# Performance work log

Hardware: AMD Instinct MI355X
Metric: run time of the kernel (lower is better)

The kernel has to match this reference:

```python
import jax, jax.numpy as jnp
import numpy as np

_CODESZ = 8   # E8 codeword dimension
_OFFSET = 0.25  # half-integer shift applied to D8 points


def _build_grid():
    # Faithful replication of get_grid(): cartesian product of arange(-4,4)
    # over 8 dims (torch.cartesian_prod order == 'ij' meshgrid, last dim fastest),
    # keep points with even coordinate sum and squared norm <= 10 (D8 subset),
    # then concat [d8 - 1/4, d8 + 1/4]. Yields 55650 codewords of dim 8.
    rng = np.arange(-4, 4, dtype=np.int8)
    pts = np.stack(np.meshgrid(*([rng] * _CODESZ), indexing='ij'), axis=-1).reshape(-1, _CODESZ)
    s = pts.sum(axis=-1, dtype=np.int16)
    n2 = (pts.astype(np.int16) * pts).sum(axis=-1)  # max 8*16 fits int16
    d8 = pts[(s % 2 == 0) & (n2 <= 10)].astype(np.float32)  # [27825, 8]
    grid = np.concatenate([d8 - _OFFSET, d8 + _OFFSET], axis=0)  # [55650, 8]
    grid_norm = (grid * grid).sum(axis=-1)  # diag(grid @ grid.T), [55650]
    return jnp.asarray(grid), jnp.asarray(grid_norm)


def setup_inputs() -> dict:
    key = jax.random.key(0)
    X = jax.random.normal(key, (8192, _CODESZ), dtype=jnp.float32)
    grid, grid_norm = _build_grid()
    return {"X": X, "grid": grid, "grid_norm": grid_norm}


def reference(X, grid, grid_norm):
    # quantize(X, return_idx=True):
    # nearest codeword under L2 <=> argmax of 2*X@g - ||g||^2
    scores = 2.0 * (X @ grid.T) - grid_norm          # [N, 55650]
    idx = jnp.argmax(scores, axis=-1)                # [N]
    vals = jnp.take(grid, idx, axis=0)               # [N, 8]
    idx_i16 = (idx + (-2 ** 15)).astype(jnp.int16)   # idx_offset + int16 cast
    return vals, idx_i16
```

## Files before the change

### kernel.cpp

```cpp
#include <hip/hip_runtime.h>
#include <math.h>


typedef short short8 __attribute__((ext_vector_type(8)));
typedef float f32x16 __attribute__((ext_vector_type(16)));

constexpr int NROWS  = 8192;
constexpr int NCW    = 55650;
constexpr int NT     = 1740;
constexpr int NCWP   = NT * 32;
constexpr int NCHUNK = 32;
constexpr int RBLK   = 32;

constexpr size_t OFF_GB = 0;
constexpr size_t OFF_XS = OFF_GB + (size_t)NCWP * 32;
constexpr size_t OFF_BK = OFF_XS + (size_t)NROWS * 64;

__device__ inline unsigned short bf16_rne(float f) {
  unsigned int u = __float_as_uint(f);
  unsigned int r = u + 0x7FFFu + ((u >> 16) & 1u);
  return (unsigned short)(r >> 16);
}
__device__ inline float bf16_f(unsigned short h) {
  return __uint_as_float(((unsigned int)h) << 16);
}
__device__ inline unsigned int enc_ord(float f) {
  unsigned int u = __float_as_uint(f);
  return (u & 0x80000000u) ? ~u : (u | 0x80000000u);
}
__device__ inline float dec_ord(unsigned int e) {
  unsigned int u = (e & 0x80000000u) ? (e & 0x7FFFFFFFu) : ~e;
  return __uint_as_float(u);
}
__device__ inline float max16(const f32x16& d) {
  float t1 = fmaxf(fmaxf(d[0], d[1]), d[2]);
  float t2 = fmaxf(fmaxf(d[3], d[4]), d[5]);
  float t3 = fmaxf(fmaxf(d[6], d[7]), d[8]);
  float t4 = fmaxf(fmaxf(d[9], d[10]), d[11]);
  float t5 = fmaxf(fmaxf(d[12], d[13]), d[14]);
  float u1 = fmaxf(fmaxf(t1, t2), t3);
  float u2 = fmaxf(fmaxf(t4, t5), d[15]);
  return fmaxf(u1, u2);
}

__global__ __launch_bounds__(256) void e8_prep(
    const float* __restrict__ X, const float* __restrict__ G,
    const float* __restrict__ GN, unsigned short* __restrict__ Gb,
    unsigned short* __restrict__ Xs, unsigned long long* __restrict__ best) {
  int i = blockIdx.x * 256 + threadIdx.x;
  if (i < NCWP) {
    unsigned short g16[16];
    if (i < NCW) {
      for (int j = 0; j < 8; ++j) g16[j] = bf16_rne(G[(size_t)i*8+j]);
      g16[8] = bf16_rne(GN[i]);
      for (int j = 9; j < 16; ++j) g16[j] = 0;
    } else {
      for (int j = 0; j < 8; ++j) g16[j] = 0;
      g16[8] = 0x7F7F;
      for (int j = 9; j < 16; ++j) g16[j] = 0;
    }
    uint4* dst = reinterpret_cast<uint4*>(Gb + (size_t)i * 16);
    dst[0] = *reinterpret_cast<uint4*>(&g16[0]);
    dst[1] = *reinterpret_cast<uint4*>(&g16[8]);
  } else if (i < NCWP + NROWS) {
    int r = i - NCWP;
    unsigned short hh[8], mm[8], ll[8], qq[8];
    for (int j = 0; j < 8; ++j) {
      float s = 2.0f * X[(size_t)r*8+j];
      unsigned short h = bf16_rne(s);  float r1 = s  - bf16_f(h);
      unsigned short m = bf16_rne(r1); float r2 = r1 - bf16_f(m);
      unsigned short l = bf16_rne(r2);
      hh[j] = h; mm[j] = m; ll[j] = l;
      qq[j] = (j == 0) ? (unsigned short)0xBF80 : 0;
    }
    uint4* dst = reinterpret_cast<uint4*>(Xs + (size_t)r * 32);
    dst[0] = *reinterpret_cast<uint4*>(hh);
    dst[1] = *reinterpret_cast<uint4*>(mm);
    dst[2] = *reinterpret_cast<uint4*>(ll);
    dst[3] = *reinterpret_cast<uint4*>(qq);
    best[r] = 0ull;
  }
}

__global__ __launch_bounds__(256, 4) void e8_main(
    const unsigned short* __restrict__ Gb,
    const unsigned short* __restrict__ Xs,
    unsigned long long* __restrict__ best) {
  const int lane = threadIdx.x & 63;
  const int wave = threadIdx.x >> 6;
  const int kg = lane >> 5, l31 = lane & 31;
  const int rowbase = blockIdx.x * 256 + wave * 64;

  short8 b10, b11, b20, b21;
  {
    const size_t row0 = (size_t)rowbase + l31;
    const size_t row1 = row0 + 32;
    b10 = *reinterpret_cast<const short8*>(Xs + (row0*4 + kg)*8);
    b20 = *reinterpret_cast<const short8*>(Xs + (row0*4 + 2 + kg)*8);
    b11 = *reinterpret_cast<const short8*>(Xs + (row1*4 + kg)*8);
    b21 = *reinterpret_cast<const short8*>(Xs + (row1*4 + 2 + kg)*8);
  }
  asm("" : "+v"(b10), "+v"(b11), "+v"(b20), "+v"(b21));

  const int ct0 = blockIdx.y * NT / NCHUNK;
  const int ct1 = (blockIdx.y + 1) * NT / NCHUNK;

  f32x16 cz;
#pragma unroll
  for (int i = 0; i < 16; ++i) cz[i] = 0.0f;

  float bs0 = -INFINITY, bs1 = -INFINITY;
  int   bi0 = 0,         bi1 = 0;

  const unsigned short* p = Gb + (size_t)ct0 * 512 + (size_t)l31 * 16;
  const int koff = kg << 3;

  short8 a1 = *reinterpret_cast<const short8*>(p);
  short8 a2 = *reinterpret_cast<const short8*>(p + koff);

  for (int ct = ct0; ct < ct1; ++ct) {
    p += 512;
    short8 na1 = *reinterpret_cast<const short8*>(p);
    short8 na2 = *reinterpret_cast<const short8*>(p + koff);

    f32x16 d0, d1;
    asm volatile(
        "v_mfma_f32_32x32x16_bf16 %0, %2, %4, %8\n\t"
        "v_mfma_f32_32x32x16_bf16 %1, %2, %5, %8\n\t"
        "v_mfma_f32_32x32x16_bf16 %0, %3, %6, %0\n\t"
        "v_mfma_f32_32x32x16_bf16 %1, %3, %7, %1\n\t"
        "s_nop 7\n\t"
        "s_nop 7"
        : "=&v"(d0), "=&v"(d1)
        : "v"(a1), "v"(a2), "v"(b10), "v"(b11), "v"(b20), "v"(b21), "v"(cz));

    const float m0 = max16(d0);
    const float m1 = max16(d1);
    bi0 = (m0 > bs0) ? ct : bi0;
    bs0 = fmaxf(bs0, m0);
    bi1 = (m1 > bs1) ? ct : bi1;
    bs1 = fmaxf(bs1, m1);
    a1 = na1; a2 = na2;
  }

  {
    unsigned long long key =
        ((unsigned long long)enc_ord(bs0) << 32) | (unsigned int)(~bi0);
    unsigned long long o = __shfl_xor(key, 32, 64);
    key = (o > key) ? o : key;
    if (lane < 32) atomicMax(&best[(size_t)rowbase + l31], key);
  }
  {
    unsigned long long key =
        ((unsigned long long)enc_ord(bs1) << 32) | (unsigned int)(~bi1);
    unsigned long long o = __shfl_xor(key, 32, 64);
    key = (o > key) ? o : key;
    if (lane < 32) atomicMax(&best[(size_t)rowbase + 32 + l31], key);
  }
}

__global__ __launch_bounds__(256) void e8_resolve(
    const unsigned short* __restrict__ Gb,
    const unsigned short* __restrict__ Xs, const float* __restrict__ G,
    const unsigned long long* __restrict__ best, float* __restrict__ out) {
  const int lane = threadIdx.x & 63;
  const int wave = threadIdx.x >> 6;
  const int kg = lane >> 5, l31 = lane & 31;
  const int rt = blockIdx.x;

  short8 b1, b2;
  {
    const size_t row = (size_t)rt * 32 + l31;
    b1 = *reinterpret_cast<const short8*>(Xs + (row*4 + kg)*8);
    b2 = *reinterpret_cast<const short8*>(Xs + (row*4 + 2 + kg)*8);
  }
  f32x16 cz;
#pragma unroll
  for (int i = 0; i < 16; ++i) cz[i] = 0.0f;

  for (int j = wave * 8; j < wave * 8 + 8; ++j) {
    const int srow = rt * 32 + j;
    const unsigned long long k = best[srow];
    const float sstar = dec_ord((unsigned int)(k >> 32));
    const int twin = (int)(~(unsigned int)(k & 0xFFFFFFFFull));

    const unsigned short* ga = Gb + (size_t)twin * 512 + (size_t)l31 * 16;
    short8 a1 = *reinterpret_cast<const short8*>(ga);
    short8 a2 = *reinterpret_cast<const short8*>(ga + (kg << 3));
    f32x16 d = __builtin_amdgcn_mfma_f32_32x32x16_bf16(a1, b1, cz, 0, 0, 0);
    d = __builtin_amdgcn_mfma_f32_32x32x16_bf16(a2, b2, d, 0, 0, 0);

    const int base = twin * 32 + 4 * kg;
    int cand = 0x7FFFFFFF;
#pragma unroll
    for (int r = 15; r >= 0; --r)
      cand = (d[r] == sstar) ? (base + ((r & 3) + 8 * (r >> 2))) : cand;
    if (l31 != j) cand = 0x7FFFFFFF;
    const int o = __shfl_xor(cand, 32, 64);
    cand = min(cand, o);
    if (lane == j) {
      const float4* g = reinterpret_cast<const float4*>(G + (size_t)cand * 8);
      float4 v0 = g[0], v1 = g[1];
      float4* od = reinterpret_cast<float4*>(out + (size_t)srow * 8);
      od[0] = v0; od[1] = v1;
      out[(size_t)NROWS * 8 + srow] = (float)(cand - 32768);
    }
  }
}

extern "C" void kernel_launch(void* const* d_in, const int* in_sizes, int n_in,
                              void* d_out, int out_size, void* d_ws, size_t ws_size,
                              hipStream_t stream) {
  const float* X  = (const float*)d_in[0];
  const float* G  = (const float*)d_in[1];
  const float* GN = (const float*)d_in[2];
  float* out = (float*)d_out;

  char* ws = (char*)d_ws;
  unsigned short*     Gb   = (unsigned short*)(ws + OFF_GB);
  unsigned short*     Xs   = (unsigned short*)(ws + OFF_XS);
  unsigned long long* best = (unsigned long long*)(ws + OFF_BK);

  e8_prep<<<(NCWP + NROWS + 255) / 256, 256, 0, stream>>>(X, G, GN, Gb, Xs, best);
  e8_main<<<dim3(RBLK, NCHUNK), 256, 0, stream>>>(Gb, Xs, best);
  e8_resolve<<<256, 256, 0, stream>>>(Gb, Xs, G, best, out);
}
```

Baseline: 46.01 us.

## Process four row tiles per wave and double-buffer codeword prefetch

Each wave now holds four 32-row X tiles instead of two, so every loaded codeword tile feeds eight MFMAs rather than four. This halves codeword loads per row. The prefetch distance grows to two tiles, and the grid is reshaped to 16 row blocks by 48 codeword chunks. The costs are higher register pressure (launch bounds drop to 3 blocks per CU) and a longer per-iteration max-reduction tail.

```diff
diff --git a/kernel.cpp b/kernel.cpp
--- a/kernel.cpp
+++ b/kernel.cpp
@@ -9,8 +9,8 @@
 constexpr int NCW    = 55650;
 constexpr int NT     = 1740;
 constexpr int NCWP   = NT * 32;
-constexpr int NCHUNK = 32;
-constexpr int RBLK   = 32;
+constexpr int NCHUNK = 48;
+constexpr int RBLK   = 16;
 
 constexpr size_t OFF_GB = 0;
 constexpr size_t OFF_XS = OFF_GB + (size_t)NCWP * 32;
@@ -82,25 +82,24 @@
   }
 }
 
-__global__ __launch_bounds__(256, 4) void e8_main(
+__global__ __launch_bounds__(256, 3) void e8_main(
     const unsigned short* __restrict__ Gb,
     const unsigned short* __restrict__ Xs,
     unsigned long long* __restrict__ best) {
   const int lane = threadIdx.x & 63;
   const int wave = threadIdx.x >> 6;
   const int kg = lane >> 5, l31 = lane & 31;
-  const int rowbase = blockIdx.x * 256 + wave * 64;
-
-  short8 b10, b11, b20, b21;
-  {
-    const size_t row0 = (size_t)rowbase + l31;
-    const size_t row1 = row0 + 32;
-    b10 = *reinterpret_cast<const short8*>(Xs + (row0*4 + kg)*8);
-    b20 = *reinterpret_cast<const short8*>(Xs + (row0*4 + 2 + kg)*8);
-    b11 = *reinterpret_cast<const short8*>(Xs + (row1*4 + kg)*8);
-    b21 = *reinterpret_cast<const short8*>(Xs + (row1*4 + 2 + kg)*8);
-  }
-  asm("" : "+v"(b10), "+v"(b11), "+v"(b20), "+v"(b21));
+  const int rowbase = blockIdx.x * 512 + wave * 128;
+
+  short8 b1f[4], b2f[4];
+#pragma unroll
+  for (int t = 0; t < 4; ++t) {
+    const size_t row = (size_t)rowbase + t * 32 + l31;
+    b1f[t] = *reinterpret_cast<const short8*>(Xs + (row*4 + kg)*8);
+    b2f[t] = *reinterpret_cast<const short8*>(Xs + (row*4 + 2 + kg)*8);
+  }
+  asm("" : "+v"(b1f[0]), "+v"(b1f[1]), "+v"(b1f[2]), "+v"(b1f[3]),
+           "+v"(b2f[0]), "+v"(b2f[1]), "+v"(b2f[2]), "+v"(b2f[3]));
 
   const int ct0 = blockIdx.y * NT / NCHUNK;
   const int ct1 = (blockIdx.y + 1) * NT / NCHUNK;
@@ -109,53 +108,60 @@
 #pragma unroll
   for (int i = 0; i < 16; ++i) cz[i] = 0.0f;
 
-  float bs0 = -INFINITY, bs1 = -INFINITY;
-  int   bi0 = 0,         bi1 = 0;
+  float bs[4] = {-INFINITY, -INFINITY, -INFINITY, -INFINITY};
+  int   bi[4] = {0, 0, 0, 0};
 
   const unsigned short* p = Gb + (size_t)ct0 * 512 + (size_t)l31 * 16;
   const int koff = kg << 3;
 
-  short8 a1 = *reinterpret_cast<const short8*>(p);
-  short8 a2 = *reinterpret_cast<const short8*>(p + koff);
+  short8 a1_0 = *reinterpret_cast<const short8*>(p);
+  short8 a2_0 = *reinterpret_cast<const short8*>(p + koff);
+  p += 512;
+  short8 a1_1 = *reinterpret_cast<const short8*>(p);
+  short8 a2_1 = *reinterpret_cast<const short8*>(p + koff);
 
   for (int ct = ct0; ct < ct1; ++ct) {
     p += 512;
     short8 na1 = *reinterpret_cast<const short8*>(p);
     short8 na2 = *reinterpret_cast<const short8*>(p + koff);
 
-    f32x16 d0, d1;
+    f32x16 d0, d1, d2, d3;
     asm volatile(
-        "v_mfma_f32_32x32x16_bf16 %0, %2, %4, %8\n\t"
-        "v_mfma_f32_32x32x16_bf16 %1, %2, %5, %8\n\t"
-        "v_mfma_f32_32x32x16_bf16 %0, %3, %6, %0\n\t"
-        "v_mfma_f32_32x32x16_bf16 %1, %3, %7, %1\n\t"
+        "v_mfma_f32_32x32x16_bf16 %0, %4, %6, %14\n\t"
+        "v_mfma_f32_32x32x16_bf16 %1, %4, %7, %14\n\t"
+        "v_mfma_f32_32x32x16_bf16 %2, %4, %8, %14\n\t"
+        "v_mfma_f32_32x32x16_bf16 %3, %4, %9, %14\n\t"
+        "v_mfma_f32_32x32x16_bf16 %0, %5, %10, %0\n\t"
+        "v_mfma_f32_32x32x16_bf16 %1, %5, %11, %1\n\t"
+        "v_mfma_f32_32x32x16_bf16 %2, %5, %12, %2\n\t"
+        "v_mfma_f32_32x32x16_bf16 %3, %5, %13, %3\n\t"
         "s_nop 7\n\t"
         "s_nop 7"
-        : "=&v"(d0), "=&v"(d1)
-        : "v"(a1), "v"(a2), "v"(b10), "v"(b11), "v"(b20), "v"(b21), "v"(cz));
+        : "=&v"(d0), "=&v"(d1), "=&v"(d2), "=&v"(d3)
+        : "v"(a1_0), "v"(a2_0),
+          "v"(b1f[0]), "v"(b1f[1]), "v"(b1f[2]), "v"(b1f[3]),
+          "v"(b2f[0]), "v"(b2f[1]), "v"(b2f[2]), "v"(b2f[3]), "v"(cz));
 
     const float m0 = max16(d0);
     const float m1 = max16(d1);
-    bi0 = (m0 > bs0) ? ct : bi0;
-    bs0 = fmaxf(bs0, m0);
-    bi1 = (m1 > bs1) ? ct : bi1;
-    bs1 = fmaxf(bs1, m1);
-    a1 = na1; a2 = na2;
-  }
-
-  {
+    const float m2 = max16(d2);
+    const float m3 = max16(d3);
+    bi[0] = (m0 > bs[0]) ? ct : bi[0];  bs[0] = fmaxf(bs[0], m0);
+    bi[1] = (m1 > bs[1]) ? ct : bi[1];  bs[1] = fmaxf(bs[1], m1);
+    bi[2] = (m2 > bs[2]) ? ct : bi[2];  bs[2] = fmaxf(bs[2], m2);
+    bi[3] = (m3 > bs[3]) ? ct : bi[3];  bs[3] = fmaxf(bs[3], m3);
+
+    a1_0 = a1_1; a2_0 = a2_1;
+    a1_1 = na1;  a2_1 = na2;
+  }
+
+#pragma unroll
+  for (int t = 0; t < 4; ++t) {
     unsigned long long key =
-        ((unsigned long long)enc_ord(bs0) << 32) | (unsigned int)(~bi0);
+        ((unsigned long long)enc_ord(bs[t]) << 32) | (unsigned int)(~bi[t]);
     unsigned long long o = __shfl_xor(key, 32, 64);
     key = (o > key) ? o : key;
-    if (lane < 32) atomicMax(&best[(size_t)rowbase + l31], key);
-  }
-  {
-    unsigned long long key =
-        ((unsigned long long)enc_ord(bs1) << 32) | (unsigned int)(~bi1);
-    unsigned long long o = __shfl_xor(key, 32, 64);
-    key = (o > key) ? o : key;
-    if (lane < 32) atomicMax(&best[(size_t)rowbase + 32 + l31], key);
+    if (lane < 32) atomicMax(&best[(size_t)rowbase + t * 32 + l31], key);
   }
 }
 
```

After: 43.56 us. -5.3%, faster.

## Defer max reduction to groups of eight tiles with elementwise max accumulators

Applied to the files above, without the earlier changes.

The main loop now keeps running elementwise maxima of the MFMA outputs across groups of eight codeword tiles and does the 16-way horizontal max and index bookkeeping once per group rather than once per tile. The resolve kernel therefore rescans all eight tiles of the winning group to find the exact codeword, and is launched with twice as many blocks, each handling half the rows. The chunk count drops from 32 to 24 and occupancy hint from 4 to 3 to fit the extra accumulator registers. This cuts VALU reduction work in the hot loop at the cost of more register pressure, fewer blocks, and more MFMA work in resolve.

```diff
diff --git a/kernel.cpp b/kernel.cpp
--- a/kernel.cpp
+++ b/kernel.cpp
@@ -9,7 +9,7 @@
 constexpr int NCW    = 55650;
 constexpr int NT     = 1740;
 constexpr int NCWP   = NT * 32;
-constexpr int NCHUNK = 32;
+constexpr int NCHUNK = 24;
 constexpr int RBLK   = 32;
 
 constexpr size_t OFF_GB = 0;
@@ -82,7 +82,35 @@
   }
 }
 
-__global__ __launch_bounds__(256, 4) void e8_main(
+#define E8_STEP(FIRST)                                                     \
+  {                                                                        \
+    p += 512;                                                              \
+    short8 na1 = *reinterpret_cast<const short8*>(p);                      \
+    short8 na2 = *reinterpret_cast<const short8*>(p + koff);               \
+    f32x16 d0, d1;                                                         \
+    asm volatile(                                                          \
+        "v_mfma_f32_32x32x16_bf16 %0, %2, %4, %8\n\t"                      \
+        "v_mfma_f32_32x32x16_bf16 %1, %2, %5, %8\n\t"                      \
+        "v_mfma_f32_32x32x16_bf16 %0, %3, %6, %0\n\t"                      \
+        "v_mfma_f32_32x32x16_bf16 %1, %3, %7, %1\n\t"                      \
+        "s_nop 7\n\t"                                                      \
+        "s_nop 7"                                                          \
+        : "=&v"(d0), "=&v"(d1)                                             \
+        : "v"(a1), "v"(a2), "v"(b10), "v"(b11), "v"(b20), "v"(b21),        \
+          "v"(cz));                                                        \
+    if (FIRST) {                                                           \
+      dm0 = d0; dm1 = d1;                                                  \
+    } else {                                                               \
+      _Pragma("unroll")                                                    \
+      for (int i = 0; i < 16; ++i) {                                       \
+        dm0[i] = fmaxf(dm0[i], d0[i]);                                     \
+        dm1[i] = fmaxf(dm1[i], d1[i]);                                     \
+      }                                                                    \
+    }                                                                      \
+    a1 = na1; a2 = na2;                                                    \
+  }
+
+__global__ __launch_bounds__(256, 3) void e8_main(
     const unsigned short* __restrict__ Gb,
     const unsigned short* __restrict__ Xs,
     unsigned long long* __restrict__ best) {
@@ -112,35 +140,30 @@
   float bs0 = -INFINITY, bs1 = -INFINITY;
   int   bi0 = 0,         bi1 = 0;
 
-  const unsigned short* p = Gb + (size_t)ct0 * 512 + (size_t)l31 * 16;
+  const unsigned short* p = Gb + (size_t)ct0 * 512 + (size_t)l31 * 16 - 512;
   const int koff = kg << 3;
 
-  short8 a1 = *reinterpret_cast<const short8*>(p);
-  short8 a2 = *reinterpret_cast<const short8*>(p + koff);
-
-  for (int ct = ct0; ct < ct1; ++ct) {
+  short8 a1, a2;
+  {
     p += 512;
-    short8 na1 = *reinterpret_cast<const short8*>(p);
-    short8 na2 = *reinterpret_cast<const short8*>(p + koff);
-
-    f32x16 d0, d1;
-    asm volatile(
-        "v_mfma_f32_32x32x16_bf16 %0, %2, %4, %8\n\t"
-        "v_mfma_f32_32x32x16_bf16 %1, %2, %5, %8\n\t"
-        "v_mfma_f32_32x32x16_bf16 %0, %3, %6, %0\n\t"
-        "v_mfma_f32_32x32x16_bf16 %1, %3, %7, %1\n\t"
-        "s_nop 7\n\t"
-        "s_nop 7"
-        : "=&v"(d0), "=&v"(d1)
-        : "v"(a1), "v"(a2), "v"(b10), "v"(b11), "v"(b20), "v"(b21), "v"(cz));
-
-    const float m0 = max16(d0);
-    const float m1 = max16(d1);
-    bi0 = (m0 > bs0) ? ct : bi0;
+    a1 = *reinterpret_cast<const short8*>(p);
+    a2 = *reinterpret_cast<const short8*>(p + koff);
+  }
+
+  int ct = ct0;
+  while (ct < ct1) {
+    const int gend = ((ct | 7) + 1 < ct1) ? (ct | 7) + 1 : ct1;
+    f32x16 dm0, dm1;
+    E8_STEP(1)
+    ++ct;
+    for (; ct < gend; ++ct) E8_STEP(0)
+    const int gid = (ct - 1) >> 3;
+    const float m0 = max16(dm0);
+    const float m1 = max16(dm1);
+    bi0 = (m0 > bs0) ? gid : bi0;
     bs0 = fmaxf(bs0, m0);
-    bi1 = (m1 > bs1) ? ct : bi1;
+    bi1 = (m1 > bs1) ? gid : bi1;
     bs1 = fmaxf(bs1, m1);
-    a1 = na1; a2 = na2;
   }
 
   {
@@ -166,7 +189,8 @@
   const int lane = threadIdx.x & 63;
   const int wave = threadIdx.x >> 6;
   const int kg = lane >> 5, l31 = lane & 31;
-  const int rt = blockIdx.x;
+  const int rt   = blockIdx.x >> 1;
+  const int half = blockIdx.x & 1;
 
   short8 b1, b2;
   {
@@ -178,23 +202,30 @@
 #pragma unroll
   for (int i = 0; i < 16; ++i) cz[i] = 0.0f;
 
-  for (int j = wave * 8; j < wave * 8 + 8; ++j) {
+  const int jbeg = half * 16 + wave * 4;
+  for (int j = jbeg; j < jbeg + 4; ++j) {
     const int srow = rt * 32 + j;
     const unsigned long long k = best[srow];
     const float sstar = dec_ord((unsigned int)(k >> 32));
-    const int twin = (int)(~(unsigned int)(k & 0xFFFFFFFFull));
-
-    const unsigned short* ga = Gb + (size_t)twin * 512 + (size_t)l31 * 16;
-    short8 a1 = *reinterpret_cast<const short8*>(ga);
-    short8 a2 = *reinterpret_cast<const short8*>(ga + (kg << 3));
-    f32x16 d = __builtin_amdgcn_mfma_f32_32x32x16_bf16(a1, b1, cz, 0, 0, 0);
-    d = __builtin_amdgcn_mfma_f32_32x32x16_bf16(a2, b2, d, 0, 0, 0);
-
-    const int base = twin * 32 + 4 * kg;
+    const int gwin = (int)(~(unsigned int)(k & 0xFFFFFFFFull));
+
+    const int t0 = gwin * 8;
+    const int t1 = (t0 + 8 < NT) ? t0 + 8 : NT;
     int cand = 0x7FFFFFFF;
+    for (int tt = t0; tt < t1; ++tt) {
+      const unsigned short* ga = Gb + (size_t)tt * 512 + (size_t)l31 * 16;
+      short8 a1 = *reinterpret_cast<const short8*>(ga);
+      short8 a2 = *reinterpret_cast<const short8*>(ga + (kg << 3));
+      f32x16 d = __builtin_amdgcn_mfma_f32_32x32x16_bf16(a1, b1, cz, 0, 0, 0);
+      d = __builtin_amdgcn_mfma_f32_32x32x16_bf16(a2, b2, d, 0, 0, 0);
+
+      int tc = 0x0FFFFFFF;
 #pragma unroll
-    for (int r = 15; r >= 0; --r)
-      cand = (d[r] == sstar) ? (base + ((r & 3) + 8 * (r >> 2))) : cand;
+      for (int r = 15; r >= 0; --r)
+        tc = (d[r] == sstar) ? ((r & 3) + 8 * (r >> 2)) : tc;
+      const int gidx = tt * 32 + 4 * kg + tc;
+      cand = (gidx < cand) ? gidx : cand;
+    }
     if (l31 != j) cand = 0x7FFFFFFF;
     const int o = __shfl_xor(cand, 32, 64);
     cand = min(cand, o);
@@ -223,5 +254,5 @@
 
   e8_prep<<<(NCWP + NROWS + 255) / 256, 256, 0, stream>>>(X, G, GN, Gb, Xs, best);
   e8_main<<<dim3(RBLK, NCHUNK), 256, 0, stream>>>(Gb, Xs, best);
-  e8_resolve<<<256, 256, 0, stream>>>(Gb, Xs, G, best, out);
-}
+  e8_resolve<<<512, 256, 0, stream>>>(Gb, Xs, G, best, out);
+}
```

Result: slower. 69.81 us (+51.7%).

## Software-pipeline MFMA with max-tracking across alternating tiles, fewer chunks

Applied to the files above, without the earlier changes.

Restructures the main loop into a two-stage ping-pong: the MFMAs for the next codeword tile are issued before the max/argmax reduction of the previous tile, with empty asm pins enforcing that order so the matrix core and VALU work overlap. Doubles the accumulator registers, so launch bounds drop from 4 to 3 waves-per-block occupancy hint. The codeword dimension is also split into 24 chunks instead of 32, giving longer loops per block and fewer atomics, at the cost of less grid parallelism. The loop still reads one tile past the chunk end, as before, which relies on the padded workspace.

```diff
diff --git a/kernel.cpp b/kernel.cpp
--- a/kernel.cpp
+++ b/kernel.cpp
@@ -9,7 +9,7 @@
 constexpr int NCW    = 55650;
 constexpr int NT     = 1740;
 constexpr int NCWP   = NT * 32;
-constexpr int NCHUNK = 32;
+constexpr int NCHUNK = 24;
 constexpr int RBLK   = 32;
 
 constexpr size_t OFF_GB = 0;
@@ -82,7 +82,33 @@
   }
 }
 
-__global__ __launch_bounds__(256, 4) void e8_main(
+#define E8_ASM(D0, D1, A1, A2)                                             \
+  asm volatile(                                                            \
+      "v_mfma_f32_32x32x16_bf16 %0, %2, %4, %8\n\t"                        \
+      "v_mfma_f32_32x32x16_bf16 %1, %2, %5, %8\n\t"                        \
+      "v_mfma_f32_32x32x16_bf16 %0, %3, %6, %0\n\t"                        \
+      "v_mfma_f32_32x32x16_bf16 %1, %3, %7, %1\n\t"                        \
+      "s_nop 7\n\t"                                                        \
+      "s_nop 7"                                                            \
+      : "=&v"(D0), "=&v"(D1)                                               \
+      : "v"(A1), "v"(A2), "v"(b10), "v"(b11), "v"(b20), "v"(b21), "v"(cz))
+
+#define E8_PIN(P0, P1, T0) asm("" : "+v"(P0), "+v"(P1) : "v"(T0))
+
+#define E8_LOAD(A1, A2)                                                    \
+  A1 = *reinterpret_cast<const short8*>(p);                                \
+  A2 = *reinterpret_cast<const short8*>(p + koff);                         \
+  p += 512;
+
+#define E8_TRACK(D0, D1, TILE)                                             \
+  {                                                                        \
+    const float m0 = max16(D0);                                            \
+    const float m1 = max16(D1);                                            \
+    bi0 = (m0 > bs0) ? (TILE) : bi0;  bs0 = fmaxf(bs0, m0);                \
+    bi1 = (m1 > bs1) ? (TILE) : bi1;  bs1 = fmaxf(bs1, m1);                \
+  }
+
+__global__ __launch_bounds__(256, 3) void e8_main(
     const unsigned short* __restrict__ Gb,
     const unsigned short* __restrict__ Xs,
     unsigned long long* __restrict__ best) {
@@ -115,32 +141,32 @@
   const unsigned short* p = Gb + (size_t)ct0 * 512 + (size_t)l31 * 16;
   const int koff = kg << 3;
 
-  short8 a1 = *reinterpret_cast<const short8*>(p);
-  short8 a2 = *reinterpret_cast<const short8*>(p + koff);
-
-  for (int ct = ct0; ct < ct1; ++ct) {
-    p += 512;
-    short8 na1 = *reinterpret_cast<const short8*>(p);
-    short8 na2 = *reinterpret_cast<const short8*>(p + koff);
-
-    f32x16 d0, d1;
-    asm volatile(
-        "v_mfma_f32_32x32x16_bf16 %0, %2, %4, %8\n\t"
-        "v_mfma_f32_32x32x16_bf16 %1, %2, %5, %8\n\t"
-        "v_mfma_f32_32x32x16_bf16 %0, %3, %6, %0\n\t"
-        "v_mfma_f32_32x32x16_bf16 %1, %3, %7, %1\n\t"
-        "s_nop 7\n\t"
-        "s_nop 7"
-        : "=&v"(d0), "=&v"(d1)
-        : "v"(a1), "v"(a2), "v"(b10), "v"(b11), "v"(b20), "v"(b21), "v"(cz));
-
-    const float m0 = max16(d0);
-    const float m1 = max16(d1);
-    bi0 = (m0 > bs0) ? ct : bi0;
-    bs0 = fmaxf(bs0, m0);
-    bi1 = (m1 > bs1) ? ct : bi1;
-    bs1 = fmaxf(bs1, m1);
-    a1 = na1; a2 = na2;
+  short8 aE1, aE2, aO1, aO2;
+  f32x16 dE0, dE1, dO0, dO1;
+
+  E8_LOAD(aE1, aE2)
+  E8_LOAD(aO1, aO2)
+  E8_ASM(dE0, dE1, aE1, aE2);
+
+  int k = ct0 + 1;
+  for (; k + 1 < ct1; k += 2) {
+    E8_LOAD(aE1, aE2)
+    E8_ASM(dO0, dO1, aO1, aO2);
+    E8_PIN(dE0, dE1, dO0);
+    E8_TRACK(dE0, dE1, k - 1)
+    E8_LOAD(aO1, aO2)
+    E8_ASM(dE0, dE1, aE1, aE2);
+    E8_PIN(dO0, dO1, dE0);
+    E8_TRACK(dO0, dO1, k)
+  }
+
+  if ((ct1 - ct0 - 1) & 1) {
+    E8_ASM(dO0, dO1, aO1, aO2);
+    E8_PIN(dE0, dE1, dO0);
+    E8_TRACK(dE0, dE1, ct1 - 2)
+    E8_TRACK(dO0, dO1, ct1 - 1)
+  } else {
+    E8_TRACK(dE0, dE1, ct1 - 1)
   }
 
   {
```

Result: faster. 43.58 us (-5.3%).
